# Kernel optimization log

Hardware: AMD Instinct MI355X
Metric: run time of the kernel (lower is better)

The kernel has to match this reference:

```python
import jax, jax.numpy as jnp
import numpy as np

D_MODEL = 1024
NUM_HEADS = 16
D_K = D_MODEL // NUM_HEADS


def setup_inputs() -> dict:
    key = jax.random.key(0)
    ks = jax.random.split(key, 11)
    B, S = 2, 2048
    scale = 1.0 / np.sqrt(D_MODEL)
    inp = {
        'q': jax.random.normal(ks[0], (B, S, D_MODEL), dtype=jnp.float32),
        'k': jax.random.normal(ks[1], (B, S, D_MODEL), dtype=jnp.float32),
        'v': jax.random.normal(ks[2], (B, S, D_MODEL), dtype=jnp.float32),
        'W_q': jax.random.normal(ks[3], (D_MODEL, D_MODEL), dtype=jnp.float32) * scale,
        'b_q': jnp.zeros((D_MODEL,), dtype=jnp.float32),
        'W_k': jax.random.normal(ks[4], (D_MODEL, D_MODEL), dtype=jnp.float32) * scale,
        'b_k': jnp.zeros((D_MODEL,), dtype=jnp.float32),
        'W_v': jax.random.normal(ks[5], (D_MODEL, D_MODEL), dtype=jnp.float32) * scale,
        'b_v': jnp.zeros((D_MODEL,), dtype=jnp.float32),
        'W_o': jax.random.normal(ks[6], (D_MODEL, D_MODEL), dtype=jnp.float32) * scale,
        'b_o': jnp.zeros((D_MODEL,), dtype=jnp.float32),
    }
    return inp


def _split_heads(x):
    # [B, S, D] -> [B, H, S, d_k]
    B, S, _ = x.shape
    return x.reshape(B, S, NUM_HEADS, D_K).transpose(0, 2, 1, 3)


def reference(q, k, v, W_q, b_q, W_k, b_k, W_v, b_v, W_o, b_o):
    # Linear projections (torch Linear: x @ W.T + b)
    qh = _split_heads(q @ W_q.T + b_q)  # [B,H,S,dk]
    kh = _split_heads(k @ W_k.T + b_k)
    vh = _split_heads(v @ W_v.T + b_v)
    scores = jnp.einsum('bhsd,bhtd->bhst', qh, kh) / jnp.sqrt(
        jnp.asarray(D_K, dtype=qh.dtype))  # [B,H,S,S]
    probs = jax.nn.softmax(scores, axis=-1)
    attn = jnp.einsum('bhst,bhtd->bhsd', probs, vh)  # [B,H,S,dk]
    B, H, S, dk = attn.shape
    combined = attn.transpose(0, 2, 1, 3).reshape(B, S, H * dk)  # [B,S,D]
    return combined @ W_o.T + b_o
```

## Files before the change

kernel.cpp:

```cpp
#include <hip/hip_runtime.h>
#include <hip/hip_bf16.h>

typedef __bf16 bf16;
typedef __attribute__((ext_vector_type(4))) __bf16 bf16x4;
typedef __attribute__((ext_vector_type(8))) __bf16 bf16x8;
typedef __attribute__((ext_vector_type(4))) float f32x4;

#define AS1C(p) ((const __attribute__((address_space(1))) void*)(p))
#define AS3(p)  ((__attribute__((address_space(3))) void*)(p))

static constexpr int B_ = 2, S_ = 2048, DM = 1024, H_ = 16, DK = 64;
static constexpr int M_ = B_ * S_;
static constexpr int NW = DM * DM;
static constexpr int NX = M_ * DM;
static constexpr float QSCL = 0.125f * 1.44269504088896340736f;

__global__ __launch_bounds__(256) void cast_all(
    const float* Wq, const float* Wk, const float* Wv, const float* Wo,
    const float* q, const float* k, const float* v,
    bf16* wq, bf16* wk, bf16* wv, bf16* wo,
    bf16* qo, bf16* ko, bf16* vo)
{
  const int z = blockIdx.y;
  const float* in; bf16* out; int n; float s = 1.f;
  switch (z) {
    case 0: in = Wq; out = wq; n = NW; s = QSCL; break;
    case 1: in = Wk; out = wk; n = NW; break;
    case 2: in = Wv; out = wv; n = NW; break;
    case 3: in = Wo; out = wo; n = NW; break;
    case 4: in = q;  out = qo; n = NX; break;
    case 5: in = k;  out = ko; n = NX; break;
    default: in = v; out = vo; n = NX; break;
  }
  const int i = (blockIdx.x * 256 + threadIdx.x) * 8;
  if (i >= n) return;
  f32x4 a = *(const f32x4*)(in + i);
  f32x4 b = *(const f32x4*)(in + i + 4);
  bf16x8 o;
#pragma unroll
  for (int j = 0; j < 4; ++j) { o[j] = (bf16)(a[j] * s); o[4 + j] = (bf16)(b[j] * s); }
  *(bf16x8*)(out + i) = o;
}

__global__ __launch_bounds__(256) void cast_f32_bf16(
    const float* __restrict__ in, bf16* __restrict__ out, int n)
{
  const int i = (blockIdx.x * 256 + threadIdx.x) * 8;
  if (i >= n) return;
  f32x4 a = *(const f32x4*)(in + i);
  f32x4 b = *(const f32x4*)(in + i + 4);
  bf16x8 o;
#pragma unroll
  for (int j = 0; j < 4; ++j) { o[j] = (bf16)a[j]; o[4 + j] = (bf16)b[j]; }
  *(bf16x8*)(out + i) = o;
}

#define BK 32

template<int WTM, bool A_BF16, bool OUT_F32>
__device__ __forceinline__ void gemm_body(
    const void* __restrict__ Ain, const bf16* __restrict__ W,
    const float* __restrict__ bias, float bscale, void* __restrict__ Cout,
    int M, int N, int K, int bx, int by)
{
  constexpr int BMt = 2 * WTM;
  constexpr int WI  = WTM / 16;
  __shared__ bf16 As[BMt * BK];
  __shared__ bf16 Bs[128 * BK];

  const int tid  = threadIdx.x;
  const int wave = tid >> 6, lane = tid & 63;
  const int quad = lane >> 4, l16 = lane & 15;
  const int wm = wave >> 1, wn = wave & 1;
  const int row0 = by * BMt;
  const int col0 = bx * 128;

  const int srow  = lane >> 2;
  const int skcol = (lane & 3) * 8;

  f32x4 acc[WI][4] = {};

  for (int k0 = 0; k0 < K; k0 += BK) {
    if constexpr (A_BF16) {
      const bf16* A = (const bf16*)Ain;
#pragma unroll
      for (int c = wave; c < BMt / 16; c += 4)
        __builtin_amdgcn_global_load_lds(
            AS1C(A + (size_t)(row0 + c * 16 + srow) * K + k0 + skcol),
            AS3(As + c * 16 * BK), 16, 0, 0);
    } else {
      const float* A = (const float*)Ain;
#pragma unroll
      for (int p = 0; p < BMt / 32; ++p) {
        const int idx = p * 256 + tid;
        const int row = idx >> 3, kc = idx & 7;
        f32x4 v = *(const f32x4*)(A + (size_t)(row0 + row) * K + k0 + kc * 4);
        bf16x4 o;
#pragma unroll
        for (int j = 0; j < 4; ++j) o[j] = (bf16)v[j];
        *(bf16x4*)(As + row * BK + kc * 4) = o;
      }
    }
#pragma unroll
    for (int i = 0; i < 2; ++i) {
      const int c = wave * 2 + i;
      __builtin_amdgcn_global_load_lds(
          AS1C(W + (size_t)(col0 + c * 16 + srow) * K + k0 + skcol),
          AS3(Bs + c * 16 * BK), 16, 0, 0);
    }
    __syncthreads();

    bf16x8 a[WI], b[4];
#pragma unroll
    for (int i = 0; i < WI; ++i)
      a[i] = *(const bf16x8*)(As + (wm * WTM + i * 16 + l16) * BK + quad * 8);
#pragma unroll
    for (int j = 0; j < 4; ++j)
      b[j] = *(const bf16x8*)(Bs + (wn * 64 + j * 16 + l16) * BK + quad * 8);

#pragma unroll
    for (int i = 0; i < WI; ++i)
#pragma unroll
      for (int j = 0; j < 4; ++j)
        acc[i][j] = __builtin_amdgcn_mfma_f32_16x16x32_bf16(a[i], b[j], acc[i][j], 0, 0, 0);
    __syncthreads();
  }

#pragma unroll
  for (int j = 0; j < 4; ++j) {
    const int col = col0 + wn * 64 + j * 16 + l16;
    const float bv = bias[col] * bscale;
#pragma unroll
    for (int i = 0; i < WI; ++i) {
#pragma unroll
      for (int r = 0; r < 4; ++r) {
        const int row = row0 + wm * WTM + i * 16 + quad * 4 + r;
        const float val = acc[i][j][r] + bv;
        if constexpr (OUT_F32)
          ((float*)Cout)[(size_t)row * N + col] = val;
        else
          ((bf16*)Cout)[(size_t)row * N + col] = (bf16)val;
      }
    }
  }
}

template<int WTM, bool A_BF16, bool OUT_F32>
__global__ __launch_bounds__(256) void gemm_bt(
    const void* __restrict__ Ain, const bf16* __restrict__ W,
    const float* __restrict__ bias, void* __restrict__ Cout,
    int M, int N, int K)
{
  gemm_body<WTM, A_BF16, OUT_F32>(Ain, W, bias, 1.0f, Cout, M, N, K,
                                  blockIdx.x, blockIdx.y);
}

template<bool A_BF16>
__global__ __launch_bounds__(256) void gemm_qkv(
    const void* A0, const void* A1, const void* A2,
    const bf16* __restrict__ Wc,
    const float* b0, const float* b1, const float* b2,
    bf16* C0, bf16* C1, bf16* C2, int M, int N, int K)
{
  const int z = blockIdx.z;
  const void* A = z == 0 ? A0 : (z == 1 ? A1 : A2);
  const float* bias = z == 0 ? b0 : (z == 1 ? b1 : b2);
  const float bscale = z == 0 ? QSCL : 1.0f;
  bf16* C = z == 0 ? C0 : (z == 1 ? C1 : C2);
  gemm_body<64, A_BF16, false>(A, Wc + (size_t)z * NW, bias, bscale, C, M, N, K,
                               blockIdx.x, blockIdx.y);
}

__global__ __launch_bounds__(256, 4) void attn_kernel(
    const bf16* __restrict__ Q, const bf16* __restrict__ Kb,
    const bf16* __restrict__ Vb, bf16* __restrict__ O)
{
  __shared__ bf16 Kt[64 * 72];
  __shared__ bf16 Vt[64 * 72];
  __shared__ bf16 Ps[4 * 16 * 72];

  const int tid  = threadIdx.x;
  const int wave = tid >> 6, lane = tid & 63;
  const int quad = lane >> 4, l16 = lane & 15;
  const int b = blockIdx.z, h = blockIdx.y;
  const int q0 = blockIdx.x * 64 + wave * 16;
  const size_t base = (size_t)b * S_ * DM + (size_t)h * DK;

  bf16x8 qf[2];
#pragma unroll
  for (int kt = 0; kt < 2; ++kt)
    qf[kt] = *(const bf16x8*)(Q + base + (size_t)(q0 + l16) * DM + kt * 32 + quad * 8);

  const bool kside = (wave < 2);
  const int ktok = tid >> 1, khalf = tid & 1;
  const int vtg = (tid - 128) >> 3, voct = tid & 7;
  const int vsw = (vtg * 4) ^ (voct * 8);

  bf16x8 st[4];
  if (kside) {
    const bf16* p = Kb + base + (size_t)ktok * DM + khalf * 32;
#pragma unroll
    for (int c = 0; c < 4; ++c) st[c] = *(const bf16x8*)(p + c * 8);
  } else {
    const bf16* p = Vb + base + (size_t)(vtg * 4) * DM + voct * 8;
#pragma unroll
    for (int i = 0; i < 4; ++i) st[i] = *(const bf16x8*)(p + (size_t)i * DM);
  }

  float l_s = 0.f;
  f32x4 accO[4] = {};
  bf16* Pw = Ps + wave * 16 * 72;

  for (int it = 0; it < S_ / 64; ++it) {
    __syncthreads();
    if (kside) {
#pragma unroll
      for (int c = 0; c < 4; ++c)
        *(bf16x8*)(Kt + ktok * 72 + khalf * 32 + c * 8) = st[c];
    } else {
#pragma unroll
      for (int j = 0; j < 8; ++j) {
        bf16x4 w = {st[0][j], st[1][j], st[2][j], st[3][j]};
        *(bf16x4*)(Vt + (voct * 8 + j) * 72 + vsw) = w;
      }
    }
    __syncthreads();

    const int kvn = ((it + 1) * 64) & (S_ - 1);
    if (kside) {
      const bf16* p = Kb + base + (size_t)(kvn + ktok) * DM + khalf * 32;
#pragma unroll
      for (int c = 0; c < 4; ++c) st[c] = *(const bf16x8*)(p + c * 8);
    } else {
      const bf16* p = Vb + base + (size_t)(kvn + vtg * 4) * DM + voct * 8;
#pragma unroll
      for (int i = 0; i < 4; ++i) st[i] = *(const bf16x8*)(p + (size_t)i * DM);
    }

    f32x4 sc[4];
#pragma unroll
    for (int ct = 0; ct < 4; ++ct) {
      const bf16* kp = Kt + (ct * 16 + l16) * 72 + quad * 8;
      f32x4 a = {0.f, 0.f, 0.f, 0.f};
      a = __builtin_amdgcn_mfma_f32_16x16x32_bf16(*(const bf16x8*)kp,        qf[0], a, 0, 0, 0);
      a = __builtin_amdgcn_mfma_f32_16x16x32_bf16(*(const bf16x8*)(kp + 32), qf[1], a, 0, 0, 0);
      sc[ct] = a;
    }

#pragma unroll
    for (int ct = 0; ct < 4; ++ct) {
      bf16x4 pk;
#pragma unroll
      for (int r = 0; r < 4; ++r) {
        const float p = exp2f(sc[ct][r]);
        l_s += p;
        pk[r] = (bf16)p;
      }
      *(bf16x4*)(Pw + l16 * 72 + ct * 16 + quad * 4) = pk;
    }
    bf16x8 pf0 = *(const bf16x8*)(Pw + l16 * 72 + quad * 8);
    bf16x8 pf1 = *(const bf16x8*)(Pw + l16 * 72 + 32 + quad * 8);

#pragma unroll
    for (int dt = 0; dt < 4; ++dt) {
      const int drow = dt * 16 + l16;
      const bf16* vp = Vt + drow * 72;
      const int sw = (drow >> 3) * 8;
      accO[dt] = __builtin_amdgcn_mfma_f32_16x16x32_bf16(
          *(const bf16x8*)(vp + ((quad * 8) ^ sw)),        pf0, accO[dt], 0, 0, 0);
      accO[dt] = __builtin_amdgcn_mfma_f32_16x16x32_bf16(
          *(const bf16x8*)(vp + ((32 + quad * 8) ^ sw)),   pf1, accO[dt], 0, 0, 0);
    }
  }

  l_s += __shfl_xor(l_s, 16, 64);
  l_s += __shfl_xor(l_s, 32, 64);
  const float inv = 1.0f / l_s;
#pragma unroll
  for (int dt = 0; dt < 4; ++dt) {
    bf16x4 o;
#pragma unroll
    for (int r = 0; r < 4; ++r) o[r] = (bf16)(accO[dt][r] * inv);
    *(bf16x4*)(O + base + (size_t)(q0 + l16) * DM + dt * 16 + quad * 4) = o;
  }
}

extern "C" void kernel_launch(void* const* d_in, const int* in_sizes, int n_in,
                              void* d_out, int out_size, void* d_ws, size_t ws_size,
                              hipStream_t stream) {
  (void)in_sizes; (void)n_in; (void)out_size;
  const float* q  = (const float*)d_in[0];
  const float* k  = (const float*)d_in[1];
  const float* v  = (const float*)d_in[2];
  const float* Wq = (const float*)d_in[3];
  const float* bq = (const float*)d_in[4];
  const float* Wk = (const float*)d_in[5];
  const float* bk = (const float*)d_in[6];
  const float* Wv = (const float*)d_in[7];
  const float* bvv= (const float*)d_in[8];
  const float* Wo = (const float*)d_in[9];
  const float* bo = (const float*)d_in[10];
  float* out = (float*)d_out;

  char* ws = (char*)d_ws;
  const size_t MB = 1024 * 1024;
  bf16* Qb  = (bf16*)(ws);
  bf16* Kbf = (bf16*)(ws + 8 * MB);
  bf16* Vbf = (bf16*)(ws + 16 * MB);
  bf16* Ab  = (bf16*)(ws + 24 * MB);
  bf16* Wc  = Ab;

  const bool big = ws_size >= 58 * MB;
  bf16* qc  = (bf16*)(ws + 32 * MB);
  bf16* kc  = (bf16*)(ws + 40 * MB);
  bf16* vc  = (bf16*)(ws + 48 * MB);
  bf16* WoC = big ? (bf16*)(ws + 56 * MB) : Qb;

  dim3 bb(256, 1, 1);
  dim3 gqkv(DM / 128, M_ / 128, 3);
  dim3 gout(DM / 128, M_ / 64, 1);

  if (big) {
    cast_all<<<dim3(NX / 2048, 7, 1), bb, 0, stream>>>(
        Wq, Wk, Wv, Wo, q, k, v,
        Wc, Wc + NW, Wc + 2 * NW, WoC, qc, kc, vc);
    gemm_qkv<true><<<gqkv, bb, 0, stream>>>(qc, kc, vc, Wc, bq, bk, bvv,
                                            Qb, Kbf, Vbf, M_, DM, DM);
  } else {
    cast_all<<<dim3(NW / 2048, 3, 1), bb, 0, stream>>>(
        Wq, Wk, Wv, Wo, q, k, v,
        Wc, Wc + NW, Wc + 2 * NW, WoC, nullptr, nullptr, nullptr);
    gemm_qkv<false><<<gqkv, bb, 0, stream>>>(q, k, v, Wc, bq, bk, bvv,
                                             Qb, Kbf, Vbf, M_, DM, DM);
  }

  attn_kernel<<<dim3(S_ / 64, H_, B_), bb, 0, stream>>>(Qb, Kbf, Vbf, Ab);

  if (!big)
    cast_f32_bf16<<<dim3(NW / 2048, 1, 1), bb, 0, stream>>>(Wo, WoC, NW);
  gemm_bt<32, true, true><<<gout, bb, 0, stream>>>(Ab, WoC, bo, out, M_, DM, DM);
}
```

Measured before the change: 246.4 us.

## Write V transposed from projection GEMM, widen GEMM K-step, use fast exp2

The V projection epilogue now writes V in a per-head transposed [B,H,DK,S] layout, so the attention kernel can stage V tiles into shared memory with plain vector copies instead of an in-register transpose and swizzle. The GEMM body loads two 32-wide K slices per barrier pair, halving synchronizations per K. The softmax uses the hardware exp2 builtin and per-register partial sums for the row denominator. The risks are strided 8-byte transposed stores in the V epilogue, doubled GEMM LDS use, and possible bank conflicts on the now unswizzled V reads.

```diff
diff --git a/kernel.cpp b/kernel.cpp
--- a/kernel.cpp
+++ b/kernel.cpp
@@ -14,6 +14,14 @@
 static constexpr int NW = DM * DM;
 static constexpr int NX = M_ * DM;
 static constexpr float QSCL = 0.125f * 1.44269504088896340736f;
+
+__device__ __forceinline__ float fast_exp2(float x) {
+#if __has_builtin(__builtin_amdgcn_exp2f)
+  return __builtin_amdgcn_exp2f(x);
+#else
+  return exp2f(x);
+#endif
+}
 
 __global__ __launch_bounds__(256) void cast_all(
     const float* Wq, const float* Wk, const float* Wv, const float* Wo,
@@ -55,18 +63,16 @@
   *(bf16x8*)(out + i) = o;
 }
 
-#define BK 32
-
 template<int WTM, bool A_BF16, bool OUT_F32>
 __device__ __forceinline__ void gemm_body(
     const void* __restrict__ Ain, const bf16* __restrict__ W,
     const float* __restrict__ bias, float bscale, void* __restrict__ Cout,
-    int M, int N, int K, int bx, int by)
+    bool transv, int M, int N, int K, int bx, int by)
 {
   constexpr int BMt = 2 * WTM;
   constexpr int WI  = WTM / 16;
-  __shared__ bf16 As[BMt * BK];
-  __shared__ bf16 Bs[128 * BK];
+  __shared__ bf16 As[2 * BMt * 32];
+  __shared__ bf16 Bs[2 * 128 * 32];
 
   const int tid  = threadIdx.x;
   const int wave = tid >> 6, lane = tid & 63;
@@ -80,49 +86,55 @@
 
   f32x4 acc[WI][4] = {};
 
-  for (int k0 = 0; k0 < K; k0 += BK) {
-    if constexpr (A_BF16) {
-      const bf16* A = (const bf16*)Ain;
-#pragma unroll
-      for (int c = wave; c < BMt / 16; c += 4)
+  for (int k0 = 0; k0 < K; k0 += 64) {
+#pragma unroll
+    for (int hf = 0; hf < 2; ++hf) {
+      const int kb = k0 + hf * 32;
+      if constexpr (A_BF16) {
+        const bf16* A = (const bf16*)Ain;
+#pragma unroll
+        for (int c = wave; c < BMt / 16; c += 4)
+          __builtin_amdgcn_global_load_lds(
+              AS1C(A + (size_t)(row0 + c * 16 + srow) * K + kb + skcol),
+              AS3(As + hf * BMt * 32 + c * 16 * 32), 16, 0, 0);
+      } else {
+        const float* A = (const float*)Ain;
+#pragma unroll
+        for (int p = 0; p < BMt / 32; ++p) {
+          const int idx = p * 256 + tid;
+          const int row = idx >> 3, kc = idx & 7;
+          f32x4 v = *(const f32x4*)(A + (size_t)(row0 + row) * K + kb + kc * 4);
+          bf16x4 o;
+#pragma unroll
+          for (int j = 0; j < 4; ++j) o[j] = (bf16)v[j];
+          *(bf16x4*)(As + hf * BMt * 32 + row * 32 + kc * 4) = o;
+        }
+      }
+#pragma unroll
+      for (int i = 0; i < 2; ++i) {
+        const int c = wave * 2 + i;
         __builtin_amdgcn_global_load_lds(
-            AS1C(A + (size_t)(row0 + c * 16 + srow) * K + k0 + skcol),
-            AS3(As + c * 16 * BK), 16, 0, 0);
-    } else {
-      const float* A = (const float*)Ain;
-#pragma unroll
-      for (int p = 0; p < BMt / 32; ++p) {
-        const int idx = p * 256 + tid;
-        const int row = idx >> 3, kc = idx & 7;
-        f32x4 v = *(const f32x4*)(A + (size_t)(row0 + row) * K + k0 + kc * 4);
-        bf16x4 o;
-#pragma unroll
-        for (int j = 0; j < 4; ++j) o[j] = (bf16)v[j];
-        *(bf16x4*)(As + row * BK + kc * 4) = o;
-      }
-    }
-#pragma unroll
-    for (int i = 0; i < 2; ++i) {
-      const int c = wave * 2 + i;
-      __builtin_amdgcn_global_load_lds(
-          AS1C(W + (size_t)(col0 + c * 16 + srow) * K + k0 + skcol),
-          AS3(Bs + c * 16 * BK), 16, 0, 0);
+            AS1C(W + (size_t)(col0 + c * 16 + srow) * K + kb + skcol),
+            AS3(Bs + hf * 128 * 32 + c * 16 * 32), 16, 0, 0);
+      }
     }
     __syncthreads();
 
-    bf16x8 a[WI], b[4];
-#pragma unroll
-    for (int i = 0; i < WI; ++i)
-      a[i] = *(const bf16x8*)(As + (wm * WTM + i * 16 + l16) * BK + quad * 8);
-#pragma unroll
-    for (int j = 0; j < 4; ++j)
-      b[j] = *(const bf16x8*)(Bs + (wn * 64 + j * 16 + l16) * BK + quad * 8);
-
-#pragma unroll
-    for (int i = 0; i < WI; ++i)
+#pragma unroll
+    for (int hf = 0; hf < 2; ++hf) {
+      bf16x8 a[WI], bfr[4];
+#pragma unroll
+      for (int i = 0; i < WI; ++i)
+        a[i] = *(const bf16x8*)(As + hf * BMt * 32 + (wm * WTM + i * 16 + l16) * 32 + quad * 8);
 #pragma unroll
       for (int j = 0; j < 4; ++j)
-        acc[i][j] = __builtin_amdgcn_mfma_f32_16x16x32_bf16(a[i], b[j], acc[i][j], 0, 0, 0);
+        bfr[j] = *(const bf16x8*)(Bs + hf * 128 * 32 + (wn * 64 + j * 16 + l16) * 32 + quad * 8);
+#pragma unroll
+      for (int i = 0; i < WI; ++i)
+#pragma unroll
+        for (int j = 0; j < 4; ++j)
+          acc[i][j] = __builtin_amdgcn_mfma_f32_16x16x32_bf16(a[i], bfr[j], acc[i][j], 0, 0, 0);
+    }
     __syncthreads();
   }
 
@@ -130,16 +142,29 @@
   for (int j = 0; j < 4; ++j) {
     const int col = col0 + wn * 64 + j * 16 + l16;
     const float bv = bias[col] * bscale;
-#pragma unroll
-    for (int i = 0; i < WI; ++i) {
-#pragma unroll
-      for (int r = 0; r < 4; ++r) {
-        const int row = row0 + wm * WTM + i * 16 + quad * 4 + r;
-        const float val = acc[i][j][r] + bv;
-        if constexpr (OUT_F32)
-          ((float*)Cout)[(size_t)row * N + col] = val;
-        else
-          ((bf16*)Cout)[(size_t)row * N + col] = (bf16)val;
+    if (!OUT_F32 && transv) {
+      const int hh = col >> 6, dd = col & 63;
+#pragma unroll
+      for (int i = 0; i < WI; ++i) {
+        const int row = row0 + wm * WTM + i * 16 + quad * 4;
+        const int bb2 = row >> 11, tok = row & 2047;
+        bf16x4 o;
+#pragma unroll
+        for (int r = 0; r < 4; ++r) o[r] = (bf16)(acc[i][j][r] + bv);
+        *(bf16x4*)((bf16*)Cout + (((size_t)bb2 * H_ + hh) * DK + dd) * S_ + tok) = o;
+      }
+    } else {
+#pragma unroll
+      for (int i = 0; i < WI; ++i) {
+#pragma unroll
+        for (int r = 0; r < 4; ++r) {
+          const int row = row0 + wm * WTM + i * 16 + quad * 4 + r;
+          const float val = acc[i][j][r] + bv;
+          if constexpr (OUT_F32)
+            ((float*)Cout)[(size_t)row * N + col] = val;
+          else
+            ((bf16*)Cout)[(size_t)row * N + col] = (bf16)val;
+        }
       }
     }
   }
@@ -151,7 +176,7 @@
     const float* __restrict__ bias, void* __restrict__ Cout,
     int M, int N, int K)
 {
-  gemm_body<WTM, A_BF16, OUT_F32>(Ain, W, bias, 1.0f, Cout, M, N, K,
+  gemm_body<WTM, A_BF16, OUT_F32>(Ain, W, bias, 1.0f, Cout, false, M, N, K,
                                   blockIdx.x, blockIdx.y);
 }
 
@@ -167,13 +192,13 @@
   const float* bias = z == 0 ? b0 : (z == 1 ? b1 : b2);
   const float bscale = z == 0 ? QSCL : 1.0f;
   bf16* C = z == 0 ? C0 : (z == 1 ? C1 : C2);
-  gemm_body<64, A_BF16, false>(A, Wc + (size_t)z * NW, bias, bscale, C, M, N, K,
-                               blockIdx.x, blockIdx.y);
+  gemm_body<64, A_BF16, false>(A, Wc + (size_t)z * NW, bias, bscale, C,
+                               z == 2, M, N, K, blockIdx.x, blockIdx.y);
 }
 
 __global__ __launch_bounds__(256, 4) void attn_kernel(
     const bf16* __restrict__ Q, const bf16* __restrict__ Kb,
-    const bf16* __restrict__ Vb, bf16* __restrict__ O)
+    const bf16* __restrict__ Vtg, bf16* __restrict__ O)
 {
   __shared__ bf16 Kt[64 * 72];
   __shared__ bf16 Vt[64 * 72];
@@ -184,7 +209,8 @@
   const int quad = lane >> 4, l16 = lane & 15;
   const int b = blockIdx.z, h = blockIdx.y;
   const int q0 = blockIdx.x * 64 + wave * 16;
-  const size_t base = (size_t)b * S_ * DM + (size_t)h * DK;
+  const size_t base  = (size_t)b * S_ * DM + (size_t)h * DK;
+  const size_t baseV = ((size_t)b * H_ + h) * DK * S_;
 
   bf16x8 qf[2];
 #pragma unroll
@@ -192,49 +218,33 @@
     qf[kt] = *(const bf16x8*)(Q + base + (size_t)(q0 + l16) * DM + kt * 32 + quad * 8);
 
   const bool kside = (wave < 2);
-  const int ktok = tid >> 1, khalf = tid & 1;
-  const int vtg = (tid - 128) >> 3, voct = tid & 7;
-  const int vsw = (vtg * 4) ^ (voct * 8);
+  const int srow  = kside ? (tid >> 1) : ((tid - 128) >> 1);
+  const int shalf = tid & 1;
+  const bf16* gp = kside
+      ? (Kb + base + (size_t)srow * DM + shalf * 32)
+      : (Vtg + baseV + (size_t)srow * S_ + shalf * 32);
+  const size_t gstep = kside ? (size_t)64 * DM : 64;
+  bf16* ldst = (kside ? Kt : Vt) + srow * 72 + shalf * 32;
 
   bf16x8 st[4];
-  if (kside) {
-    const bf16* p = Kb + base + (size_t)ktok * DM + khalf * 32;
-#pragma unroll
-    for (int c = 0; c < 4; ++c) st[c] = *(const bf16x8*)(p + c * 8);
-  } else {
-    const bf16* p = Vb + base + (size_t)(vtg * 4) * DM + voct * 8;
-#pragma unroll
-    for (int i = 0; i < 4; ++i) st[i] = *(const bf16x8*)(p + (size_t)i * DM);
-  }
-
-  float l_s = 0.f;
+#pragma unroll
+  for (int c = 0; c < 4; ++c) st[c] = *(const bf16x8*)(gp + c * 8);
+  gp += gstep;
+
+  f32x4 lacc = {0.f, 0.f, 0.f, 0.f};
   f32x4 accO[4] = {};
   bf16* Pw = Ps + wave * 16 * 72;
 
   for (int it = 0; it < S_ / 64; ++it) {
     __syncthreads();
-    if (kside) {
-#pragma unroll
-      for (int c = 0; c < 4; ++c)
-        *(bf16x8*)(Kt + ktok * 72 + khalf * 32 + c * 8) = st[c];
-    } else {
-#pragma unroll
-      for (int j = 0; j < 8; ++j) {
-        bf16x4 w = {st[0][j], st[1][j], st[2][j], st[3][j]};
-        *(bf16x4*)(Vt + (voct * 8 + j) * 72 + vsw) = w;
-      }
-    }
+#pragma unroll
+    for (int c = 0; c < 4; ++c) *(bf16x8*)(ldst + c * 8) = st[c];
     __syncthreads();
 
-    const int kvn = ((it + 1) * 64) & (S_ - 1);
-    if (kside) {
-      const bf16* p = Kb + base + (size_t)(kvn + ktok) * DM + khalf * 32;
-#pragma unroll
-      for (int c = 0; c < 4; ++c) st[c] = *(const bf16x8*)(p + c * 8);
-    } else {
-      const bf16* p = Vb + base + (size_t)(kvn + vtg * 4) * DM + voct * 8;
-#pragma unroll
-      for (int i = 0; i < 4; ++i) st[i] = *(const bf16x8*)(p + (size_t)i * DM);
+    if (it + 1 < S_ / 64) {
+#pragma unroll
+      for (int c = 0; c < 4; ++c) st[c] = *(const bf16x8*)(gp + c * 8);
+      gp += gstep;
     }
 
     f32x4 sc[4];
@@ -252,8 +262,8 @@
       bf16x4 pk;
 #pragma unroll
       for (int r = 0; r < 4; ++r) {
-        const float p = exp2f(sc[ct][r]);
-        l_s += p;
+        const float p = fast_exp2(sc[ct][r]);
+        lacc[r] += p;
         pk[r] = (bf16)p;
       }
       *(bf16x4*)(Pw + l16 * 72 + ct * 16 + quad * 4) = pk;
@@ -263,16 +273,15 @@
 
 #pragma unroll
     for (int dt = 0; dt < 4; ++dt) {
-      const int drow = dt * 16 + l16;
-      const bf16* vp = Vt + drow * 72;
-      const int sw = (drow >> 3) * 8;
+      const bf16* vp = Vt + (dt * 16 + l16) * 72;
       accO[dt] = __builtin_amdgcn_mfma_f32_16x16x32_bf16(
-          *(const bf16x8*)(vp + ((quad * 8) ^ sw)),        pf0, accO[dt], 0, 0, 0);
+          *(const bf16x8*)(vp + quad * 8),      pf0, accO[dt], 0, 0, 0);
       accO[dt] = __builtin_amdgcn_mfma_f32_16x16x32_bf16(
-          *(const bf16x8*)(vp + ((32 + quad * 8) ^ sw)),   pf1, accO[dt], 0, 0, 0);
-    }
-  }
-
+          *(const bf16x8*)(vp + 32 + quad * 8), pf1, accO[dt], 0, 0, 0);
+    }
+  }
+
+  float l_s = (lacc[0] + lacc[1]) + (lacc[2] + lacc[3]);
   l_s += __shfl_xor(l_s, 16, 64);
   l_s += __shfl_xor(l_s, 32, 64);
   const float inv = 1.0f / l_s;
@@ -306,7 +315,7 @@
   const size_t MB = 1024 * 1024;
   bf16* Qb  = (bf16*)(ws);
   bf16* Kbf = (bf16*)(ws + 8 * MB);
-  bf16* Vbf = (bf16*)(ws + 16 * MB);
+  bf16* Vtg = (bf16*)(ws + 16 * MB);
   bf16* Ab  = (bf16*)(ws + 24 * MB);
   bf16* Wc  = Ab;
 
@@ -325,16 +334,16 @@
         Wq, Wk, Wv, Wo, q, k, v,
         Wc, Wc + NW, Wc + 2 * NW, WoC, qc, kc, vc);
     gemm_qkv<true><<<gqkv, bb, 0, stream>>>(qc, kc, vc, Wc, bq, bk, bvv,
-                                            Qb, Kbf, Vbf, M_, DM, DM);
+                                            Qb, Kbf, Vtg, M_, DM, DM);
   } else {
     cast_all<<<dim3(NW / 2048, 3, 1), bb, 0, stream>>>(
         Wq, Wk, Wv, Wo, q, k, v,
         Wc, Wc + NW, Wc + 2 * NW, WoC, nullptr, nullptr, nullptr);
     gemm_qkv<false><<<gqkv, bb, 0, stream>>>(q, k, v, Wc, bq, bk, bvv,
-                                             Qb, Kbf, Vbf, M_, DM, DM);
-  }
-
-  attn_kernel<<<dim3(S_ / 64, H_, B_), bb, 0, stream>>>(Qb, Kbf, Vbf, Ab);
+                                             Qb, Kbf, Vtg, M_, DM, DM);
+  }
+
+  attn_kernel<<<dim3(S_ / 64, H_, B_), bb, 0, stream>>>(Qb, Kbf, Vtg, Ab);
 
   if (!big)
     cast_f32_bf16<<<dim3(NW / 2048, 1, 1), bb, 0, stream>>>(Wo, WoC, NW);
```

After: 234.0 us. 5.0% less time.
